# Optimization experiments

Measured on AMD Instinct MI355X. Metric: run time of the kernel, lower is better.

The kernel has to match this reference:

```python
import jax, jax.numpy as jnp
import numpy as np

T = 32.0                       # softmax temperature
THRESH = float(np.cos(np.pi * 40.0 / 180.0))  # cos(degree), degree=40
NEG_INF = -9.0e15


def setup_inputs() -> dict:
    key = jax.random.key(0)
    ks = jax.random.split(key, 11)
    B, C, D_IMG, D_ATT, H_ATT, H = 2048, 1000, 2048, 312, 128, 128
    def rn(k, shape, scale=1.0):
        return jax.random.normal(k, shape, dtype=jnp.float32) * scale
    return {
        "image_feats": rn(ks[0], (B, D_IMG)),
        "img_proto":   rn(ks[1], (C, D_IMG)),
        "attributes":  rn(ks[2], (C, D_ATT)),
        "unused":      0,
        # parameters
        "att_g":   rn(ks[3], (D_ATT, H_ATT), 0.05),
        "slim_w":  rn(ks[4], (D_IMG, D_ATT), 0.02),   # proto_slim weight (transposed torch layout)
        "slim_b":  rn(ks[5], (D_ATT,), 0.02),
        "img_w":   rn(ks[6], (D_IMG, H), 0.02),
        "proto_w": rn(ks[7], (2 * D_ATT, H), 0.02),   # att_dim + proto_red_dim = 624
        "proto_b": rn(ks[8], (1, H), 0.02),
        "fc_w":    rn(ks[9], (H, 1), 0.05),
        "fc_b":    rn(ks[10], (1,), 0.05),
    }


def reference(image_feats, img_proto, attributes, unused,
              att_g, slim_w, slim_b, img_w, proto_w, proto_b, fc_w, fc_b):
    # proto_slim: [C, D_img] -> [C, att_dim]
    proto_red = img_proto @ slim_w + slim_b

    # --- get_attention: cosine similarity among attribute projections ---
    g = attributes @ att_g                                   # [C, att_hC] (g == h in original)
    gn = g / jnp.clip(jnp.linalg.norm(g, axis=1, keepdims=True), 1e-12)
    sim = gn @ gn.T                                          # [C, C] cosine similarity
    raw = jnp.where(sim > THRESH, sim, NEG_INF)              # threshold mask
    attn = jax.nn.softmax(raw * T, axis=1)                   # [C, C]

    # --- propagate prototypes ---
    att_outs = attn @ attributes                             # [C, att_dim]
    img_proto_outs = attn @ proto_red                        # [C, att_dim]
    outs = jnp.concatenate([att_outs, img_proto_outs], axis=1)  # [C, 2*att_dim]

    # --- relation MLP (broadcast instead of materialized expand+matmul) ---
    img_h = image_feats @ img_w                              # [B, H]
    proto_h = outs @ proto_w                                 # [C, H]
    hidden = jax.nn.relu(img_h[:, None, :] + proto_h[None, :, :] + proto_b)  # [B, C, H]
    outputs = hidden @ fc_w + fc_b                           # [B, C, 1]
    return outputs[..., 0]                                   # [B, C]
```

## Files before the change

### kernel.cpp

```cpp
#include <hip/hip_runtime.h>

typedef unsigned short ushort_t;
typedef __bf16 bf16x8 __attribute__((ext_vector_type(8)));
typedef float f32x4 __attribute__((ext_vector_type(4)));
typedef float f32x2 __attribute__((ext_vector_type(2)));
typedef ushort_t us4 __attribute__((ext_vector_type(4)));

#define T_SOFT 32.0f
#define THRESH 0.76604444311897803f
#define SW 1048

__device__ __forceinline__ ushort_t f2bf(float f) {
  union { float f; unsigned u; } x; x.f = f;
  unsigned r = (x.u + 0x7fffu + ((x.u >> 16) & 1u)) >> 16;
  return (ushort_t)r;
}
__device__ __forceinline__ float bf2f(ushort_t h) {
  union { unsigned u; float f; } x; x.u = ((unsigned)h) << 16; return x.f;
}

__device__ __forceinline__ us4 pack4(float4 x) {
  union { unsigned u[2]; us4 h; } r;
  union { float4 f; unsigned u[4]; } a;
  a.f = x;
  r.u[0] = __builtin_amdgcn_perm(a.u[1] + 0x8000u, a.u[0] + 0x8000u, 0x07060302u);
  r.u[1] = __builtin_amdgcn_perm(a.u[3] + 0x8000u, a.u[2] + 0x8000u, 0x07060302u);
  return r.h;
}

__global__ __launch_bounds__(256) void tr3_k(const float* __restrict__ img_w, ushort_t* __restrict__ imgwT,
                                             const float* __restrict__ proto_w, ushort_t* __restrict__ protowT,
                                             const float* __restrict__ slim_w, ushort_t* __restrict__ slim_bf,
                                             const float* __restrict__ attributes, ushort_t* __restrict__ attr_bf,
                                             ushort_t* __restrict__ gn_bf,
                                             const float* __restrict__ slim_b, const float* __restrict__ proto_b,
                                             float* __restrict__ biasG) {
  int b = blockIdx.x, tid = threadIdx.x;
  if (b >= 336) {
    if (b < 496) {
      int t = (b - 336) * 256 + tid;
      int row = t / 20, c0 = (t - row * 20) * 16;
      #pragma unroll
      for (int g = 0; g < 4; ++g) {
        int c4 = c0 + g * 4;
        us4 v = {0, 0, 0, 0};
        if (c4 < 312) v = pack4(*reinterpret_cast<const float4*>(slim_w + (size_t)row * 312 + c4));
        *reinterpret_cast<us4*>(slim_bf + (size_t)row * 320 + c4) = v;
      }
    } else if (b < 576) {
      int t = (b - 496) * 256 + tid;
      int row = t / 20, c0 = (t - row * 20) * 16;
      #pragma unroll
      for (int g = 0; g < 4; ++g) {
        int c4 = c0 + g * 4;
        us4 v = {0, 0, 0, 0};
        if (row < 1000 && c4 < 312) v = pack4(*reinterpret_cast<const float4*>(attributes + (size_t)row * 312 + c4));
        *reinterpret_cast<us4*>(attr_bf + (size_t)row * 320 + c4) = v;
      }
    } else if (b == 576) {
      us4 z = {0, 0, 0, 0};
      *reinterpret_cast<us4*>(gn_bf + 1000 * 128 + tid * 4) = z;
    } else {
      int h = tid & 127;
      float acc = proto_b[h];
      for (int n = 0; n < 312; n += 4) {
        acc += slim_b[n + 0] * proto_w[(size_t)(312 + n) * 128 + h];
        acc += slim_b[n + 1] * proto_w[(size_t)(313 + n) * 128 + h];
        acc += slim_b[n + 2] * proto_w[(size_t)(314 + n) * 128 + h];
        acc += slim_b[n + 3] * proto_w[(size_t)(315 + n) * 128 + h];
      }
      if (tid < 128) biasG[h] = acc;
    }
    return;
  }
  __shared__ float tl[32][33];
  const float* src; ushort_t* dst; int R, C, Rpad, local;
  if (b < 256) { src = img_w;   dst = imgwT;   R = 2048; C = 128; Rpad = 2048; local = b;       }
  else         { src = proto_w; dst = protowT; R = 624;  C = 128; Rpad = 640;  local = b - 256; }
  int rt = local >> 2, ct = local & 3;
  int r0 = rt * 32, c0 = ct * 32;
  #pragma unroll
  for (int p = 0; p < 4; ++p) {
    int idx = p * 256 + tid;
    int rr = idx >> 5, cc = idx & 31;
    float v = 0.f;
    if (r0 + rr < R && c0 + cc < C) v = src[(size_t)(r0 + rr) * C + (c0 + cc)];
    tl[cc][rr] = v;
  }
  __syncthreads();
  int cc = tid >> 3, rq = tid & 7;
  us4 o;
  o[0] = f2bf(tl[cc][rq * 4 + 0]);
  o[1] = f2bf(tl[cc][rq * 4 + 1]);
  o[2] = f2bf(tl[cc][rq * 4 + 2]);
  o[3] = f2bf(tl[cc][rq * 4 + 3]);
  *reinterpret_cast<us4*>(dst + (size_t)(c0 + cc) * Rpad + r0 + rq * 4) = o;
}

__device__ __forceinline__ void gemm_imgh(const float* __restrict__ A, const ushort_t* __restrict__ BT,
                                          float* __restrict__ Cp, int r0, int k0,
                                          ushort_t* __restrict__ As, ushort_t* __restrict__ Bs, int tid) {
  const int SA = 72;
  int lane = tid & 63, wv = tid >> 6;
  int l15 = lane & 15, quad = lane >> 4;
  int arow = tid >> 4, akq = tid & 15;
  int brow = tid >> 3, bkq = tid & 7;
  const float* agp[8];
  #pragma unroll
  for (int p = 0; p < 8; ++p) agp[p] = A + (size_t)(r0 + arow + p * 16) * 2048 + k0 + akq * 4;
  const ushort_t* bgp[4];
  #pragma unroll
  for (int p = 0; p < 4; ++p) bgp[p] = BT + (size_t)(brow + p * 32) * 2048 + k0 + bkq * 8;

  float4 ap[8]; bf16x8 bp[4];
  #pragma unroll
  for (int p = 0; p < 8; ++p) ap[p] = *reinterpret_cast<const float4*>(agp[p]);
  #pragma unroll
  for (int p = 0; p < 4; ++p) bp[p] = *reinterpret_cast<const bf16x8*>(bgp[p]);

  f32x4 acc[2][8];
  #pragma unroll
  for (int i = 0; i < 2; ++i)
    #pragma unroll
    for (int j = 0; j < 8; ++j) acc[i][j] = f32x4{0.f, 0.f, 0.f, 0.f};

  for (int s = 0; s < 4; ++s) {
    if (s) __syncthreads();
    #pragma unroll
    for (int p = 0; p < 8; ++p)
      *reinterpret_cast<us4*>(As + (arow + p * 16) * SA + akq * 4) = pack4(ap[p]);
    #pragma unroll
    for (int p = 0; p < 4; ++p)
      *reinterpret_cast<bf16x8*>(Bs + (brow + p * 32) * SA + bkq * 8) = bp[p];
    if (s + 1 < 4) {
      #pragma unroll
      for (int p = 0; p < 8; ++p) ap[p] = *reinterpret_cast<const float4*>(agp[p] + 64);
      #pragma unroll
      for (int p = 0; p < 4; ++p) bp[p] = *reinterpret_cast<const bf16x8*>(bgp[p] + 64);
      #pragma unroll
      for (int p = 0; p < 8; ++p) agp[p] += 64;
      #pragma unroll
      for (int p = 0; p < 4; ++p) bgp[p] += 64;
    }
    __syncthreads();
    #pragma unroll
    for (int kh = 0; kh < 2; ++kh) {
      bf16x8 af[2];
      #pragma unroll
      for (int pi = 0; pi < 2; ++pi)
        af[pi] = *reinterpret_cast<bf16x8*>(As + ((wv * 2 + pi) * 16 + l15) * SA + kh * 32 + quad * 8);
      #pragma unroll
      for (int ct = 0; ct < 8; ++ct) {
        bf16x8 bfr = *reinterpret_cast<bf16x8*>(Bs + (ct * 16 + l15) * SA + kh * 32 + quad * 8);
        acc[0][ct] = __builtin_amdgcn_mfma_f32_16x16x32_bf16(af[0], bfr, acc[0][ct], 0, 0, 0);
        acc[1][ct] = __builtin_amdgcn_mfma_f32_16x16x32_bf16(af[1], bfr, acc[1][ct], 0, 0, 0);
      }
    }
  }
  #pragma unroll
  for (int pi = 0; pi < 2; ++pi)
    #pragma unroll
    for (int ct = 0; ct < 8; ++ct) {
      int col = ct * 16 + l15;
      #pragma unroll
      for (int r = 0; r < 4; ++r) {
        int row = r0 + (wv * 2 + pi) * 16 + quad * 4 + r;
        Cp[(size_t)row * 128 + col] = acc[pi][ct][r];
      }
    }
}

__device__ __forceinline__ void gemm_bb(const ushort_t* __restrict__ A, int sa,
                                        const ushort_t* __restrict__ B, int sb,
                                        int nsteps, ushort_t* __restrict__ As, ushort_t* __restrict__ Bs,
                                        int tid, f32x4 acc[2][8]) {
  const int SA = 72;
  int lane = tid & 63, wv = tid >> 6;
  int l15 = lane & 15, quad = lane >> 4;
  int hrow = tid >> 3, hkq = tid & 7;
  const ushort_t* ap = A + (size_t)hrow * sa + hkq * 8;
  const ushort_t* bp = B + (size_t)hrow * sb + hkq * 8;
  bf16x8 ar[4], br[4];
  #pragma unroll
  for (int p = 0; p < 4; ++p) {
    ar[p] = *reinterpret_cast<const bf16x8*>(ap + (size_t)p * 32 * sa);
    br[p] = *reinterpret_cast<const bf16x8*>(bp + (size_t)p * 32 * sb);
  }
  for (int s = 0; s < nsteps; ++s) {
    if (s) __syncthreads();
    #pragma unroll
    for (int p = 0; p < 4; ++p) {
      *reinterpret_cast<bf16x8*>(As + (hrow + p * 32) * SA + hkq * 8) = ar[p];
      *reinterpret_cast<bf16x8*>(Bs + (hrow + p * 32) * SA + hkq * 8) = br[p];
    }
    if (s + 1 < nsteps) {
      ap += 64; bp += 64;
      #pragma unroll
      for (int p = 0; p < 4; ++p) {
        ar[p] = *reinterpret_cast<const bf16x8*>(ap + (size_t)p * 32 * sa);
        br[p] = *reinterpret_cast<const bf16x8*>(bp + (size_t)p * 32 * sb);
      }
    }
    __syncthreads();
    #pragma unroll
    for (int kh = 0; kh < 2; ++kh) {
      bf16x8 af[2];
      #pragma unroll
      for (int pi = 0; pi < 2; ++pi)
        af[pi] = *reinterpret_cast<bf16x8*>(As + ((wv * 2 + pi) * 16 + l15) * SA + kh * 32 + quad * 8);
      #pragma unroll
      for (int ct = 0; ct < 8; ++ct) {
        bf16x8 bfr = *reinterpret_cast<bf16x8*>(Bs + (ct * 16 + l15) * SA + kh * 32 + quad * 8);
        acc[0][ct] = __builtin_amdgcn_mfma_f32_16x16x32_bf16(af[0], bfr, acc[0][ct], 0, 0, 0);
        acc[1][ct] = __builtin_amdgcn_mfma_f32_16x16x32_bf16(af[1], bfr, acc[1][ct], 0, 0, 0);
      }
    }
  }
}

__device__ __forceinline__ void gemm_b32(const ushort_t* __restrict__ A, int sa,
                                         const float* __restrict__ Bsrc, int sb, int brow0, int browmax,
                                         int nsteps, ushort_t* __restrict__ As, ushort_t* __restrict__ Bs,
                                         int tid, f32x4 acc[2][8]) {
  const int SA = 72;
  int lane = tid & 63, wv = tid >> 6;
  int l15 = lane & 15, quad = lane >> 4;
  int hrow = tid >> 3, hkq = tid & 7;
  int frow = tid >> 4, fkq = tid & 15;
  const ushort_t* ap = A + (size_t)hrow * sa + hkq * 8;
  const float* bgp[8];
  #pragma unroll
  for (int p = 0; p < 8; ++p) {
    int r = brow0 + frow + p * 16; if (r > browmax) r = browmax;
    bgp[p] = Bsrc + (size_t)r * sb + fkq * 4;
  }
  bf16x8 ar[4]; float4 brf[8];
  #pragma unroll
  for (int p = 0; p < 4; ++p) ar[p] = *reinterpret_cast<const bf16x8*>(ap + (size_t)p * 32 * sa);
  #pragma unroll
  for (int p = 0; p < 8; ++p) brf[p] = *reinterpret_cast<const float4*>(bgp[p]);
  for (int s = 0; s < nsteps; ++s) {
    if (s) __syncthreads();
    #pragma unroll
    for (int p = 0; p < 4; ++p)
      *reinterpret_cast<bf16x8*>(As + (hrow + p * 32) * SA + hkq * 8) = ar[p];
    #pragma unroll
    for (int p = 0; p < 8; ++p)
      *reinterpret_cast<us4*>(Bs + (frow + p * 16) * SA + fkq * 4) = pack4(brf[p]);
    if (s + 1 < nsteps) {
      ap += 64;
      #pragma unroll
      for (int p = 0; p < 4; ++p) ar[p] = *reinterpret_cast<const bf16x8*>(ap + (size_t)p * 32 * sa);
      #pragma unroll
      for (int p = 0; p < 8; ++p) { bgp[p] += 64; brf[p] = *reinterpret_cast<const float4*>(bgp[p]); }
    }
    __syncthreads();
    #pragma unroll
    for (int kh = 0; kh < 2; ++kh) {
      bf16x8 af[2];
      #pragma unroll
      for (int pi = 0; pi < 2; ++pi)
        af[pi] = *reinterpret_cast<bf16x8*>(As + ((wv * 2 + pi) * 16 + l15) * SA + kh * 32 + quad * 8);
      #pragma unroll
      for (int ct = 0; ct < 8; ++ct) {
        bf16x8 bfr = *reinterpret_cast<bf16x8*>(Bs + (ct * 16 + l15) * SA + kh * 32 + quad * 8);
        acc[0][ct] = __builtin_amdgcn_mfma_f32_16x16x32_bf16(af[0], bfr, acc[0][ct], 0, 0, 0);
        acc[1][ct] = __builtin_amdgcn_mfma_f32_16x16x32_bf16(af[1], bfr, acc[1][ct], 0, 0, 0);
      }
    }
  }
}

__global__ __launch_bounds__(256) void mega_k(
    const float* __restrict__ attributes, const float* __restrict__ att_g,
    ushort_t* __restrict__ gn_bf,
    const float* __restrict__ image_feats, const ushort_t* __restrict__ imgwT,
    float* __restrict__ ihp,
    const ushort_t* __restrict__ protowT, const ushort_t* __restrict__ slim_bf,
    ushort_t* __restrict__ M2T) {
  __shared__ ushort_t As[128 * 72];
  __shared__ ushort_t Bs[128 * 72];
  int b = blockIdx.x, tid = threadIdx.x;
  if (b < 125) {
    __shared__ float a_lds[8][316];
    __shared__ float red2[8][2];
    int h = tid & 127;
    int c0 = b * 8;
    for (int idx = tid; idx < 8 * 312; idx += 256) {
      int r = idx / 312;
      int k = idx - r * 312;
      a_lds[r][k] = attributes[(c0 + r) * 312 + k];
    }
    __syncthreads();
    float acc[8] = {0.f,0.f,0.f,0.f,0.f,0.f,0.f,0.f};
    #pragma unroll 2
    for (int k = 0; k < 312; k += 4) {
      float w0 = att_g[(k + 0) * 128 + h];
      float w1 = att_g[(k + 1) * 128 + h];
      float w2 = att_g[(k + 2) * 128 + h];
      float w3 = att_g[(k + 3) * 128 + h];
      #pragma unroll
      for (int r = 0; r < 8; ++r) {
        float4 a4 = *reinterpret_cast<const float4*>(&a_lds[r][k]);
        acc[r] += a4.x * w0 + a4.y * w1 + a4.z * w2 + a4.w * w3;
      }
    }
    int lane = tid & 63, wvid = (tid >> 6) & 1;
    #pragma unroll
    for (int r = 0; r < 8; ++r) {
      float v = acc[r] * acc[r];
      #pragma unroll
      for (int off = 32; off > 0; off >>= 1) v += __shfl_xor(v, off, 64);
      if (lane == 0) red2[r][wvid] = v;
    }
    __syncthreads();
    #pragma unroll
    for (int r = 0; r < 8; ++r) {
      float nrm = fmaxf(sqrtf(red2[r][0] + red2[r][1]), 1e-12f);
      gn_bf[(c0 + r) * 128 + h] = f2bf(acc[r] / nrm);
    }
    return;
  }
  b -= 125;
  if (b < 128) {
    int tile = b >> 3, kc = b & 7;
    gemm_imgh(image_feats, imgwT, ihp + (size_t)kc * 2048 * 128, tile * 128, kc * 256, As, Bs, tid);
    return;
  }
  b -= 128;
  int c0 = b * 128;
  f32x4 acc[2][8];
  #pragma unroll
  for (int i = 0; i < 2; ++i)
    #pragma unroll
    for (int j = 0; j < 8; ++j) acc[i][j] = f32x4{0.f, 0.f, 0.f, 0.f};
  gemm_bb(protowT + 312, 640, slim_bf + (size_t)c0 * 320, 320, 5, As, Bs, tid, acc);
  int lane = tid & 63, wv = tid >> 6;
  int l15 = lane & 15, quad = lane >> 4;
  #pragma unroll
  for (int pi = 0; pi < 2; ++pi)
    #pragma unroll
    for (int ct = 0; ct < 8; ++ct) {
      int col = c0 + ct * 16 + l15;
      #pragma unroll
      for (int r = 0; r < 4; ++r) {
        int row = (wv * 2 + pi) * 16 + quad * 4 + r;
        M2T[(size_t)row * 2048 + col] = f2bf(acc[pi][ct][r]);
      }
    }
}

__global__ __launch_bounds__(256) void k3_k(
    const float* __restrict__ ihp, float* __restrict__ img_h,
    const ushort_t* __restrict__ protowT, const ushort_t* __restrict__ M2T,
    const ushort_t* __restrict__ attr_bf, const float* __restrict__ img_proto,
    float* __restrict__ GT_part) {
  __shared__ ushort_t As[128 * 72];
  __shared__ ushort_t Bs[128 * 72];
  int b = blockIdx.x, tid = threadIdx.x;
  if (b < 64) {
    int t = b * 256 + tid;
    size_t base = (size_t)t * 16;
    #pragma unroll
    for (int g = 0; g < 4; ++g) {
      float4 s = *reinterpret_cast<const float4*>(ihp + base + g * 4);
      #pragma unroll
      for (int c = 1; c < 8; ++c) {
        float4 v = *reinterpret_cast<const float4*>(ihp + (size_t)c * 262144 + base + g * 4);
        s.x += v.x; s.y += v.y; s.z += v.z; s.w += v.w;
      }
      *reinterpret_cast<float4*>(img_h + base + g * 4) = s;
    }
    return;
  }
  int q = b - 64;
  int jt = q / 5, ch = q - jt * 5;
  int j0 = jt * 128;
  f32x4 acc[2][8];
  #pragma unroll
  for (int i = 0; i < 2; ++i)
    #pragma unroll
    for (int j = 0; j < 8; ++j) acc[i][j] = f32x4{0.f, 0.f, 0.f, 0.f};
  if (ch == 0) {
    gemm_bb(protowT, 640, attr_bf + (size_t)j0 * 320, 320, 5, As, Bs, tid, acc);
  } else {
    int k0 = (ch - 1) * 512;
    gemm_b32(M2T + k0, 2048, img_proto + k0, 2048, j0, 999, 8, As, Bs, tid, acc);
  }
  int lane = tid & 63, wv = tid >> 6;
  int l15 = lane & 15, quad = lane >> 4;
  float* dst = GT_part + (size_t)ch * 128 * 1024;
  #pragma unroll
  for (int pi = 0; pi < 2; ++pi)
    #pragma unroll
    for (int ct = 0; ct < 8; ++ct) {
      int col = j0 + ct * 16 + l15;
      #pragma unroll
      for (int r = 0; r < 4; ++r) {
        int row = (wv * 2 + pi) * 16 + quad * 4 + r;
        dst[(size_t)row * 1024 + col] = acc[pi][ct][r];
      }
    }
}

__global__ __launch_bounds__(256) void k4_k(const float* __restrict__ GT_part,
                                            const float* __restrict__ biasG,
                                            ushort_t* __restrict__ GT) {
  int t = blockIdx.x * 256 + threadIdx.x;
  size_t base = (size_t)t * 16;
  int row = (int)(base >> 10);
  float bg = biasG[row];
  #pragma unroll
  for (int g = 0; g < 4; ++g) {
    float4 s = *reinterpret_cast<const float4*>(GT_part + base + g * 4);
    #pragma unroll
    for (int c = 1; c < 5; ++c) {
      float4 v = *reinterpret_cast<const float4*>(GT_part + (size_t)c * 131072 + base + g * 4);
      s.x += v.x; s.y += v.y; s.z += v.z; s.w += v.w;
    }
    s.x += bg; s.y += bg; s.z += bg; s.w += bg;
    *reinterpret_cast<us4*>(GT + base + g * 4) = pack4(s);
  }
}

__global__ __launch_bounds__(256) void attn5_k(
    const ushort_t* __restrict__ gn_bf, const ushort_t* __restrict__ GT,
    float* __restrict__ ph) {
  __shared__ ushort_t W[16 * SW];
  __shared__ float rsum[16];
  __shared__ int flags[63];
  int tid = threadIdx.x;
  int i0 = blockIdx.x * 16;
  int lane = tid & 63, wv = tid >> 6;
  int l15 = lane & 15, quad = lane >> 4;
  if (tid < 63) flags[tid] = 0;
  if (tid >= 64 && tid < 80) rsum[tid - 64] = 0.f;
  W[(tid >> 4) * SW + 1008 + (tid & 15)] = 0;
  __syncthreads();

  const ushort_t* abase = gn_bf + (size_t)(i0 + l15) * 128 + quad * 8;
  bf16x8 af0 = *reinterpret_cast<const bf16x8*>(abase);
  bf16x8 af1 = *reinterpret_cast<const bf16x8*>(abase + 32);
  bf16x8 af2 = *reinterpret_cast<const bf16x8*>(abase + 64);
  bf16x8 af3 = *reinterpret_cast<const bf16x8*>(abase + 96);
  float rs[4] = {0.f, 0.f, 0.f, 0.f};
  for (int jt = wv; jt < 63; jt += 4) {
    const ushort_t* bbase = gn_bf + (size_t)(jt * 16 + l15) * 128 + quad * 8;
    f32x4 d = {0.f, 0.f, 0.f, 0.f};
    d = __builtin_amdgcn_mfma_f32_16x16x32_bf16(af0, *reinterpret_cast<const bf16x8*>(bbase),      d, 0, 0, 0);
    d = __builtin_amdgcn_mfma_f32_16x16x32_bf16(af1, *reinterpret_cast<const bf16x8*>(bbase + 32), d, 0, 0, 0);
    d = __builtin_amdgcn_mfma_f32_16x16x32_bf16(af2, *reinterpret_cast<const bf16x8*>(bbase + 64), d, 0, 0, 0);
    d = __builtin_amdgcn_mfma_f32_16x16x32_bf16(af3, *reinterpret_cast<const bf16x8*>(bbase + 96), d, 0, 0, 0);
    int hot = 0;
    #pragma unroll
    for (int r = 0; r < 4; ++r) {
      float w = 0.f;
      if (d[r] > THRESH) { w = __expf(T_SOFT * (d[r] - 1.0f)); hot = 1; }
      ushort_t wb = f2bf(w);
      W[(quad * 4 + r) * SW + jt * 16 + l15] = wb;
      rs[r] += bf2f(wb);
    }
    if (hot) flags[jt] = 1;
  }
  #pragma unroll
  for (int r = 0; r < 4; ++r) {
    float v = rs[r];
    v += __shfl_xor(v, 1, 64); v += __shfl_xor(v, 2, 64);
    v += __shfl_xor(v, 4, 64); v += __shfl_xor(v, 8, 64);
    if (l15 == 0) atomicAdd(&rsum[quad * 4 + r], v);
  }
  __syncthreads();

  f32x4 acc2[2];
  acc2[0] = f32x4{0.f, 0.f, 0.f, 0.f};
  acc2[1] = f32x4{0.f, 0.f, 0.f, 0.f};
  for (int s = 0; s < 32; ++s) {
    int f = flags[2 * s] | ((2 * s + 1 < 63) ? flags[2 * s + 1] : 0);
    if (!f) continue;
    bf16x8 a = *reinterpret_cast<bf16x8*>(W + l15 * SW + s * 32 + quad * 8);
    #pragma unroll
    for (int t = 0; t < 2; ++t) {
      int h = (wv * 2 + t) * 16 + l15;
      bf16x8 bfr = *reinterpret_cast<const bf16x8*>(GT + (size_t)h * 1024 + s * 32 + quad * 8);
      acc2[t] = __builtin_amdgcn_mfma_f32_16x16x32_bf16(a, bfr, acc2[t], 0, 0, 0);
    }
  }
  #pragma unroll
  for (int t = 0; t < 2; ++t) {
    int h = (wv * 2 + t) * 16 + l15;
    #pragma unroll
    for (int r = 0; r < 4; ++r) {
      int row = quad * 4 + r;
      int gi = i0 + row;
      float inv = 1.f / fmaxf(rsum[row], 1e-30f);
      if (gi < 1000) ph[(size_t)gi * 128 + h] = acc2[t][r] * inv;
    }
  }
}

__global__ __launch_bounds__(512) void final_k(
    const float* __restrict__ img_h, const float* __restrict__ ph,
    const float* __restrict__ fc_w, const float* __restrict__ fc_b,
    float* __restrict__ out) {
  __shared__ float ih[128][132];
  __shared__ float ps[64][132];
  __shared__ float ws_[128];
  int tid = threadIdx.x;
  int b0 = blockIdx.x * 128;
  int c0 = blockIdx.y * 64;
  for (int idx = tid; idx < 4096; idx += 512) {
    int row = idx >> 5, c4 = (idx & 31) * 4;
    float4 v = *reinterpret_cast<const float4*>(img_h + (size_t)(b0 + row) * 128 + c4);
    *reinterpret_cast<float4*>(&ih[row][c4]) = v;
  }
  for (int idx = tid; idx < 2048; idx += 512) {
    int row = idx >> 5, c4 = (idx & 31) * 4;
    int c = c0 + row;
    float4 v = make_float4(0.f, 0.f, 0.f, 0.f);
    if (c < 1000) v = *reinterpret_cast<const float4*>(ph + (size_t)c * 128 + c4);
    *reinterpret_cast<float4*>(&ps[row][c4]) = v;
  }
  if (tid < 128) ws_[tid] = fc_w[tid];
  __syncthreads();
  int tx = tid & 15, ty = tid >> 4;
  f32x2 acc[4][4] = {};
  const f32x2 zero2 = {0.f, 0.f};
  for (int h = 0; h < 128; h += 4) {
    float4 w4 = *reinterpret_cast<float4*>(&ws_[h]);
    f32x2 wlo = {w4.x, w4.y}, whi = {w4.z, w4.w};
    float4 a4[4], p4[4];
    #pragma unroll
    for (int i = 0; i < 4; ++i) a4[i] = *reinterpret_cast<float4*>(&ih[ty * 4 + i][h]);
    #pragma unroll
    for (int j = 0; j < 4; ++j) p4[j] = *reinterpret_cast<float4*>(&ps[tx * 4 + j][h]);
    #pragma unroll
    for (int i = 0; i < 4; ++i) {
      f32x2 alo = {a4[i].x, a4[i].y}, ahi = {a4[i].z, a4[i].w};
      #pragma unroll
      for (int j = 0; j < 4; ++j) {
        f32x2 plo = {p4[j].x, p4[j].y}, phi = {p4[j].z, p4[j].w};
        f32x2 t0 = __builtin_elementwise_max(alo + plo, zero2);
        f32x2 t1 = __builtin_elementwise_max(ahi + phi, zero2);
        acc[i][j] = acc[i][j] + t0 * wlo;
        acc[i][j] = acc[i][j] + t1 * whi;
      }
    }
  }
  float fb = fc_b[0];
  #pragma unroll
  for (int i = 0; i < 4; ++i) {
    int b = b0 + ty * 4 + i;
    int c = c0 + tx * 4;
    if (c < 1000) {
      float4 v = make_float4(acc[i][0].x + acc[i][0].y + fb, acc[i][1].x + acc[i][1].y + fb,
                             acc[i][2].x + acc[i][2].y + fb, acc[i][3].x + acc[i][3].y + fb);
      *reinterpret_cast<float4*>(out + (size_t)b * 1000 + c) = v;
    }
  }
}

extern "C" void kernel_launch(void* const* d_in, const int* in_sizes, int n_in,
                              void* d_out, int out_size, void* d_ws, size_t ws_size,
                              hipStream_t stream) {
  const float* image_feats = (const float*)d_in[0];
  const float* img_proto   = (const float*)d_in[1];
  const float* attributes  = (const float*)d_in[2];
  const float* att_g   = (const float*)d_in[4];
  const float* slim_w  = (const float*)d_in[5];
  const float* slim_b  = (const float*)d_in[6];
  const float* img_w   = (const float*)d_in[7];
  const float* proto_w = (const float*)d_in[8];
  const float* proto_b = (const float*)d_in[9];
  const float* fc_w    = (const float*)d_in[10];
  const float* fc_b    = (const float*)d_in[11];
  float* out = (float*)d_out;

  char* ws = (char*)d_ws;
  size_t o = 0;
  auto alloc = [&](size_t bytes) { size_t r = o; o += (bytes + 255) & ~(size_t)255; return r; };
  ushort_t* imgwT   = (ushort_t*)(ws + alloc(128ull * 2048 * 2));
  ushort_t* protowT = (ushort_t*)(ws + alloc(128ull * 640 * 2));
  ushort_t* slim_bf = (ushort_t*)(ws + alloc(2048ull * 320 * 2));
  ushort_t* attr_bf = (ushort_t*)(ws + alloc(1024ull * 320 * 2));
  ushort_t* gn_bf   = (ushort_t*)(ws + alloc(1008ull * 128 * 2));
  ushort_t* M2T     = (ushort_t*)(ws + alloc(128ull * 2048 * 2));
  ushort_t* GT      = (ushort_t*)(ws + alloc(128ull * 1024 * 2));
  float* biasG     = (float*)(ws + alloc(128ull * 4));
  float* ihp       = (float*)(ws + alloc(8ull * 2048 * 128 * 4));
  float* GT_part   = (float*)(ws + alloc(5ull * 128 * 1024 * 4));
  float* img_h     = (float*)(ws + alloc(2048ull * 128 * 4));
  float* ph        = (float*)(ws + alloc(1000ull * 128 * 4));

  tr3_k<<<578, 256, 0, stream>>>(img_w, imgwT, proto_w, protowT, slim_w, slim_bf,
                                 attributes, attr_bf, gn_bf, slim_b, proto_b, biasG);

  mega_k<<<269, 256, 0, stream>>>(attributes, att_g, gn_bf,
                                  image_feats, imgwT, ihp, protowT, slim_bf, M2T);

  k3_k<<<104, 256, 0, stream>>>(ihp, img_h, protowT, M2T, attr_bf, img_proto, GT_part);

  k4_k<<<32, 256, 0, stream>>>(GT_part, biasG, GT);

  attn5_k<<<63, 256, 0, stream>>>(gn_bf, GT, ph);

  final_k<<<dim3(16, 16), 512, 0, stream>>>(img_h, ph, fc_w, fc_b, out);
}
```

Baseline: 169.9 us.

## Fold weight transpose/convert into GEMM staging and drop the separate prep kernel

Removes the standalone transpose/bf16 conversion kernel by having each GEMM convert fp32 weights and activations to bf16 while staging them into shared memory. The attributes@proto_w GEMM moves into the first kernel, and the partial-sum grids of the reduction kernel are reshaped. The attention kernel goes to 512 threads with one MFMA tile per wave, and the final kernel uses smaller 256-thread blocks for more parallelism. This saves a launch and the intermediate bf16 copies, at the cost of redoing the fp32-to-bf16 conversion inside each GEMM block, including strided transposed loads.

Measured after the change: 169.0 us. Within noise of the previous version (-0.5%).

```diff
diff --git a/kernel.cpp b/kernel.cpp
--- a/kernel.cpp
+++ b/kernel.cpp
@@ -9,6 +9,7 @@
 #define T_SOFT 32.0f
 #define THRESH 0.76604444311897803f
 #define SW 1048
+#define SA 72
 
 __device__ __forceinline__ ushort_t f2bf(float f) {
   union { float f; unsigned u; } x; x.f = f;
@@ -28,258 +29,84 @@
   return r.h;
 }
 
-__global__ __launch_bounds__(256) void tr3_k(const float* __restrict__ img_w, ushort_t* __restrict__ imgwT,
-                                             const float* __restrict__ proto_w, ushort_t* __restrict__ protowT,
-                                             const float* __restrict__ slim_w, ushort_t* __restrict__ slim_bf,
-                                             const float* __restrict__ attributes, ushort_t* __restrict__ attr_bf,
-                                             ushort_t* __restrict__ gn_bf,
-                                             const float* __restrict__ slim_b, const float* __restrict__ proto_b,
-                                             float* __restrict__ biasG) {
-  int b = blockIdx.x, tid = threadIdx.x;
-  if (b >= 336) {
-    if (b < 496) {
-      int t = (b - 336) * 256 + tid;
-      int row = t / 20, c0 = (t - row * 20) * 16;
-      #pragma unroll
-      for (int g = 0; g < 4; ++g) {
-        int c4 = c0 + g * 4;
-        us4 v = {0, 0, 0, 0};
-        if (c4 < 312) v = pack4(*reinterpret_cast<const float4*>(slim_w + (size_t)row * 312 + c4));
-        *reinterpret_cast<us4*>(slim_bf + (size_t)row * 320 + c4) = v;
-      }
-    } else if (b < 576) {
-      int t = (b - 496) * 256 + tid;
-      int row = t / 20, c0 = (t - row * 20) * 16;
-      #pragma unroll
-      for (int g = 0; g < 4; ++g) {
-        int c4 = c0 + g * 4;
-        us4 v = {0, 0, 0, 0};
-        if (row < 1000 && c4 < 312) v = pack4(*reinterpret_cast<const float4*>(attributes + (size_t)row * 312 + c4));
-        *reinterpret_cast<us4*>(attr_bf + (size_t)row * 320 + c4) = v;
-      }
-    } else if (b == 576) {
-      us4 z = {0, 0, 0, 0};
-      *reinterpret_cast<us4*>(gn_bf + 1000 * 128 + tid * 4) = z;
-    } else {
-      int h = tid & 127;
-      float acc = proto_b[h];
-      for (int n = 0; n < 312; n += 4) {
-        acc += slim_b[n + 0] * proto_w[(size_t)(312 + n) * 128 + h];
-        acc += slim_b[n + 1] * proto_w[(size_t)(313 + n) * 128 + h];
-        acc += slim_b[n + 2] * proto_w[(size_t)(314 + n) * 128 + h];
-        acc += slim_b[n + 3] * proto_w[(size_t)(315 + n) * 128 + h];
-      }
-      if (tid < 128) biasG[h] = acc;
-    }
-    return;
-  }
-  __shared__ float tl[32][33];
-  const float* src; ushort_t* dst; int R, C, Rpad, local;
-  if (b < 256) { src = img_w;   dst = imgwT;   R = 2048; C = 128; Rpad = 2048; local = b;       }
-  else         { src = proto_w; dst = protowT; R = 624;  C = 128; Rpad = 640;  local = b - 256; }
-  int rt = local >> 2, ct = local & 3;
-  int r0 = rt * 32, c0 = ct * 32;
-  #pragma unroll
-  for (int p = 0; p < 4; ++p) {
-    int idx = p * 256 + tid;
-    int rr = idx >> 5, cc = idx & 31;
-    float v = 0.f;
-    if (r0 + rr < R && c0 + cc < C) v = src[(size_t)(r0 + rr) * C + (c0 + cc)];
-    tl[cc][rr] = v;
-  }
-  __syncthreads();
-  int cc = tid >> 3, rq = tid & 7;
-  us4 o;
-  o[0] = f2bf(tl[cc][rq * 4 + 0]);
-  o[1] = f2bf(tl[cc][rq * 4 + 1]);
-  o[2] = f2bf(tl[cc][rq * 4 + 2]);
-  o[3] = f2bf(tl[cc][rq * 4 + 3]);
-  *reinterpret_cast<us4*>(dst + (size_t)(c0 + cc) * Rpad + r0 + rq * 4) = o;
-}
-
-__device__ __forceinline__ void gemm_imgh(const float* __restrict__ A, const ushort_t* __restrict__ BT,
-                                          float* __restrict__ Cp, int r0, int k0,
-                                          ushort_t* __restrict__ As, ushort_t* __restrict__ Bs, int tid) {
-  const int SA = 72;
+__device__ __forceinline__ void stage_T(const float* __restrict__ src, int srs, int rbase, int rlimit,
+                                        int nbase, ushort_t* __restrict__ dst, int tid) {
+  int kg = (tid >> 4) * 4;
+  int ns = (tid & 15) * 8;
+  float v[4][8];
+  #pragma unroll
+  for (int i = 0; i < 4; ++i) {
+    int r = rbase + kg + i;
+    float4 a = make_float4(0.f,0.f,0.f,0.f), c = make_float4(0.f,0.f,0.f,0.f);
+    if (r < rlimit) {
+      a = *reinterpret_cast<const float4*>(src + (size_t)r * srs + nbase + ns);
+      c = *reinterpret_cast<const float4*>(src + (size_t)r * srs + nbase + ns + 4);
+    }
+    v[i][0]=a.x; v[i][1]=a.y; v[i][2]=a.z; v[i][3]=a.w;
+    v[i][4]=c.x; v[i][5]=c.y; v[i][6]=c.z; v[i][7]=c.w;
+  }
+  #pragma unroll
+  for (int j = 0; j < 8; ++j) {
+    us4 o;
+    o[0] = f2bf(v[0][j]); o[1] = f2bf(v[1][j]); o[2] = f2bf(v[2][j]); o[3] = f2bf(v[3][j]);
+    *reinterpret_cast<us4*>(dst + (size_t)(ns + j) * SA + kg) = o;
+  }
+}
+
+__device__ __forceinline__ void stage_R(const float* __restrict__ src, int srs, int rowbase, int rowmax,
+                                        int kbase, int climit, ushort_t* __restrict__ dst, int tid) {
+  int frow = tid >> 4;
+  int fk = (tid & 15) * 4;
+  #pragma unroll
+  for (int p = 0; p < 8; ++p) {
+    int row = rowbase + frow + p * 16; if (row > rowmax) row = rowmax;
+    int k = kbase + fk;
+    float4 val = make_float4(0.f,0.f,0.f,0.f);
+    if (k < climit) val = *reinterpret_cast<const float4*>(src + (size_t)row * srs + k);
+    *reinterpret_cast<us4*>(dst + (size_t)(frow + p * 16) * SA + fk) = pack4(val);
+  }
+}
+
+__device__ __forceinline__ void stage_Abf(const ushort_t* __restrict__ src, int srs, int kbase,
+                                          ushort_t* __restrict__ dst, int tid) {
+  int hrow = tid >> 3;
+  int hk = (tid & 7) * 8;
+  #pragma unroll
+  for (int p = 0; p < 4; ++p)
+    *reinterpret_cast<bf16x8*>(dst + (size_t)(hrow + p * 32) * SA + hk) =
+      *reinterpret_cast<const bf16x8*>(src + (size_t)(hrow + p * 32) * srs + kbase + hk);
+}
+
+__device__ __forceinline__ void mfma8(ushort_t* __restrict__ As, ushort_t* __restrict__ Bs,
+                                      int tid, f32x4 acc[2][8]) {
   int lane = tid & 63, wv = tid >> 6;
   int l15 = lane & 15, quad = lane >> 4;
-  int arow = tid >> 4, akq = tid & 15;
-  int brow = tid >> 3, bkq = tid & 7;
-  const float* agp[8];
-  #pragma unroll
-  for (int p = 0; p < 8; ++p) agp[p] = A + (size_t)(r0 + arow + p * 16) * 2048 + k0 + akq * 4;
-  const ushort_t* bgp[4];
-  #pragma unroll
-  for (int p = 0; p < 4; ++p) bgp[p] = BT + (size_t)(brow + p * 32) * 2048 + k0 + bkq * 8;
-
-  float4 ap[8]; bf16x8 bp[4];
-  #pragma unroll
-  for (int p = 0; p < 8; ++p) ap[p] = *reinterpret_cast<const float4*>(agp[p]);
-  #pragma unroll
-  for (int p = 0; p < 4; ++p) bp[p] = *reinterpret_cast<const bf16x8*>(bgp[p]);
-
-  f32x4 acc[2][8];
-  #pragma unroll
-  for (int i = 0; i < 2; ++i)
-    #pragma unroll
-    for (int j = 0; j < 8; ++j) acc[i][j] = f32x4{0.f, 0.f, 0.f, 0.f};
-
-  for (int s = 0; s < 4; ++s) {
-    if (s) __syncthreads();
-    #pragma unroll
-    for (int p = 0; p < 8; ++p)
-      *reinterpret_cast<us4*>(As + (arow + p * 16) * SA + akq * 4) = pack4(ap[p]);
-    #pragma unroll
-    for (int p = 0; p < 4; ++p)
-      *reinterpret_cast<bf16x8*>(Bs + (brow + p * 32) * SA + bkq * 8) = bp[p];
-    if (s + 1 < 4) {
-      #pragma unroll
-      for (int p = 0; p < 8; ++p) ap[p] = *reinterpret_cast<const float4*>(agp[p] + 64);
-      #pragma unroll
-      for (int p = 0; p < 4; ++p) bp[p] = *reinterpret_cast<const bf16x8*>(bgp[p] + 64);
-      #pragma unroll
-      for (int p = 0; p < 8; ++p) agp[p] += 64;
-      #pragma unroll
-      for (int p = 0; p < 4; ++p) bgp[p] += 64;
-    }
-    __syncthreads();
-    #pragma unroll
-    for (int kh = 0; kh < 2; ++kh) {
-      bf16x8 af[2];
-      #pragma unroll
-      for (int pi = 0; pi < 2; ++pi)
-        af[pi] = *reinterpret_cast<bf16x8*>(As + ((wv * 2 + pi) * 16 + l15) * SA + kh * 32 + quad * 8);
-      #pragma unroll
-      for (int ct = 0; ct < 8; ++ct) {
-        bf16x8 bfr = *reinterpret_cast<bf16x8*>(Bs + (ct * 16 + l15) * SA + kh * 32 + quad * 8);
-        acc[0][ct] = __builtin_amdgcn_mfma_f32_16x16x32_bf16(af[0], bfr, acc[0][ct], 0, 0, 0);
-        acc[1][ct] = __builtin_amdgcn_mfma_f32_16x16x32_bf16(af[1], bfr, acc[1][ct], 0, 0, 0);
-      }
-    }
-  }
-  #pragma unroll
-  for (int pi = 0; pi < 2; ++pi)
+  #pragma unroll
+  for (int kh = 0; kh < 2; ++kh) {
+    bf16x8 af[2];
+    #pragma unroll
+    for (int pi = 0; pi < 2; ++pi)
+      af[pi] = *reinterpret_cast<bf16x8*>(As + ((wv * 2 + pi) * 16 + l15) * SA + kh * 32 + quad * 8);
     #pragma unroll
     for (int ct = 0; ct < 8; ++ct) {
-      int col = ct * 16 + l15;
-      #pragma unroll
-      for (int r = 0; r < 4; ++r) {
-        int row = r0 + (wv * 2 + pi) * 16 + quad * 4 + r;
-        Cp[(size_t)row * 128 + col] = acc[pi][ct][r];
-      }
-    }
-}
-
-__device__ __forceinline__ void gemm_bb(const ushort_t* __restrict__ A, int sa,
-                                        const ushort_t* __restrict__ B, int sb,
-                                        int nsteps, ushort_t* __restrict__ As, ushort_t* __restrict__ Bs,
-                                        int tid, f32x4 acc[2][8]) {
-  const int SA = 72;
-  int lane = tid & 63, wv = tid >> 6;
-  int l15 = lane & 15, quad = lane >> 4;
-  int hrow = tid >> 3, hkq = tid & 7;
-  const ushort_t* ap = A + (size_t)hrow * sa + hkq * 8;
-  const ushort_t* bp = B + (size_t)hrow * sb + hkq * 8;
-  bf16x8 ar[4], br[4];
-  #pragma unroll
-  for (int p = 0; p < 4; ++p) {
-    ar[p] = *reinterpret_cast<const bf16x8*>(ap + (size_t)p * 32 * sa);
-    br[p] = *reinterpret_cast<const bf16x8*>(bp + (size_t)p * 32 * sb);
-  }
-  for (int s = 0; s < nsteps; ++s) {
-    if (s) __syncthreads();
-    #pragma unroll
-    for (int p = 0; p < 4; ++p) {
-      *reinterpret_cast<bf16x8*>(As + (hrow + p * 32) * SA + hkq * 8) = ar[p];
-      *reinterpret_cast<bf16x8*>(Bs + (hrow + p * 32) * SA + hkq * 8) = br[p];
-    }
-    if (s + 1 < nsteps) {
-      ap += 64; bp += 64;
-      #pragma unroll
-      for (int p = 0; p < 4; ++p) {
-        ar[p] = *reinterpret_cast<const bf16x8*>(ap + (size_t)p * 32 * sa);
-        br[p] = *reinterpret_cast<const bf16x8*>(bp + (size_t)p * 32 * sb);
-      }
-    }
-    __syncthreads();
-    #pragma unroll
-    for (int kh = 0; kh < 2; ++kh) {
-      bf16x8 af[2];
-      #pragma unroll
-      for (int pi = 0; pi < 2; ++pi)
-        af[pi] = *reinterpret_cast<bf16x8*>(As + ((wv * 2 + pi) * 16 + l15) * SA + kh * 32 + quad * 8);
-      #pragma unroll
-      for (int ct = 0; ct < 8; ++ct) {
-        bf16x8 bfr = *reinterpret_cast<bf16x8*>(Bs + (ct * 16 + l15) * SA + kh * 32 + quad * 8);
-        acc[0][ct] = __builtin_amdgcn_mfma_f32_16x16x32_bf16(af[0], bfr, acc[0][ct], 0, 0, 0);
-        acc[1][ct] = __builtin_amdgcn_mfma_f32_16x16x32_bf16(af[1], bfr, acc[1][ct], 0, 0, 0);
-      }
-    }
-  }
-}
-
-__device__ __forceinline__ void gemm_b32(const ushort_t* __restrict__ A, int sa,
-                                         const float* __restrict__ Bsrc, int sb, int brow0, int browmax,
-                                         int nsteps, ushort_t* __restrict__ As, ushort_t* __restrict__ Bs,
-                                         int tid, f32x4 acc[2][8]) {
-  const int SA = 72;
-  int lane = tid & 63, wv = tid >> 6;
-  int l15 = lane & 15, quad = lane >> 4;
-  int hrow = tid >> 3, hkq = tid & 7;
-  int frow = tid >> 4, fkq = tid & 15;
-  const ushort_t* ap = A + (size_t)hrow * sa + hkq * 8;
-  const float* bgp[8];
-  #pragma unroll
-  for (int p = 0; p < 8; ++p) {
-    int r = brow0 + frow + p * 16; if (r > browmax) r = browmax;
-    bgp[p] = Bsrc + (size_t)r * sb + fkq * 4;
-  }
-  bf16x8 ar[4]; float4 brf[8];
-  #pragma unroll
-  for (int p = 0; p < 4; ++p) ar[p] = *reinterpret_cast<const bf16x8*>(ap + (size_t)p * 32 * sa);
-  #pragma unroll
-  for (int p = 0; p < 8; ++p) brf[p] = *reinterpret_cast<const float4*>(bgp[p]);
-  for (int s = 0; s < nsteps; ++s) {
-    if (s) __syncthreads();
-    #pragma unroll
-    for (int p = 0; p < 4; ++p)
-      *reinterpret_cast<bf16x8*>(As + (hrow + p * 32) * SA + hkq * 8) = ar[p];
-    #pragma unroll
-    for (int p = 0; p < 8; ++p)
-      *reinterpret_cast<us4*>(Bs + (frow + p * 16) * SA + fkq * 4) = pack4(brf[p]);
-    if (s + 1 < nsteps) {
-      ap += 64;
-      #pragma unroll
-      for (int p = 0; p < 4; ++p) ar[p] = *reinterpret_cast<const bf16x8*>(ap + (size_t)p * 32 * sa);
-      #pragma unroll
-      for (int p = 0; p < 8; ++p) { bgp[p] += 64; brf[p] = *reinterpret_cast<const float4*>(bgp[p]); }
-    }
-    __syncthreads();
-    #pragma unroll
-    for (int kh = 0; kh < 2; ++kh) {
-      bf16x8 af[2];
-      #pragma unroll
-      for (int pi = 0; pi < 2; ++pi)
-        af[pi] = *reinterpret_cast<bf16x8*>(As + ((wv * 2 + pi) * 16 + l15) * SA + kh * 32 + quad * 8);
-      #pragma unroll
-      for (int ct = 0; ct < 8; ++ct) {
-        bf16x8 bfr = *reinterpret_cast<bf16x8*>(Bs + (ct * 16 + l15) * SA + kh * 32 + quad * 8);
-        acc[0][ct] = __builtin_amdgcn_mfma_f32_16x16x32_bf16(af[0], bfr, acc[0][ct], 0, 0, 0);
-        acc[1][ct] = __builtin_amdgcn_mfma_f32_16x16x32_bf16(af[1], bfr, acc[1][ct], 0, 0, 0);
-      }
-    }
-  }
-}
-
-__global__ __launch_bounds__(256) void mega_k(
+      bf16x8 bfr = *reinterpret_cast<bf16x8*>(Bs + (ct * 16 + l15) * SA + kh * 32 + quad * 8);
+      acc[0][ct] = __builtin_amdgcn_mfma_f32_16x16x32_bf16(af[0], bfr, acc[0][ct], 0, 0, 0);
+      acc[1][ct] = __builtin_amdgcn_mfma_f32_16x16x32_bf16(af[1], bfr, acc[1][ct], 0, 0, 0);
+    }
+  }
+}
+
+__global__ __launch_bounds__(256) void prep_k(
     const float* __restrict__ attributes, const float* __restrict__ att_g,
     ushort_t* __restrict__ gn_bf,
-    const float* __restrict__ image_feats, const ushort_t* __restrict__ imgwT,
+    const float* __restrict__ image_feats, const float* __restrict__ img_w,
     float* __restrict__ ihp,
-    const ushort_t* __restrict__ protowT, const ushort_t* __restrict__ slim_bf,
-    ushort_t* __restrict__ M2T) {
-  __shared__ ushort_t As[128 * 72];
-  __shared__ ushort_t Bs[128 * 72];
+    const float* __restrict__ proto_w, const float* __restrict__ slim_w,
+    ushort_t* __restrict__ M2T, float* __restrict__ GT_part,
+    const float* __restrict__ slim_b, const float* __restrict__ proto_b,
+    float* __restrict__ biasG) {
+  __shared__ ushort_t As[128 * SA];
+  __shared__ ushort_t Bs[128 * SA];
   int b = blockIdx.x, tid = threadIdx.x;
   if (b < 125) {
     __shared__ float a_lds[8][316];
@@ -321,48 +148,113 @@
     }
     return;
   }
-  b -= 125;
-  if (b < 128) {
-    int tile = b >> 3, kc = b & 7;
-    gemm_imgh(image_feats, imgwT, ihp + (size_t)kc * 2048 * 128, tile * 128, kc * 256, As, Bs, tid);
-    return;
-  }
-  b -= 128;
-  int c0 = b * 128;
-  f32x4 acc[2][8];
-  #pragma unroll
-  for (int i = 0; i < 2; ++i)
-    #pragma unroll
-    for (int j = 0; j < 8; ++j) acc[i][j] = f32x4{0.f, 0.f, 0.f, 0.f};
-  gemm_bb(protowT + 312, 640, slim_bf + (size_t)c0 * 320, 320, 5, As, Bs, tid, acc);
+  if (b == 125) {
+    us4 z = {0, 0, 0, 0};
+    *reinterpret_cast<us4*>(gn_bf + 1000 * 128 + tid * 4) = z;
+    return;
+  }
+  if (b == 126) {
+    int h = tid & 127;
+    float acc = proto_b[h];
+    for (int n = 0; n < 312; n += 4) {
+      acc += slim_b[n + 0] * proto_w[(size_t)(312 + n) * 128 + h];
+      acc += slim_b[n + 1] * proto_w[(size_t)(313 + n) * 128 + h];
+      acc += slim_b[n + 2] * proto_w[(size_t)(314 + n) * 128 + h];
+      acc += slim_b[n + 3] * proto_w[(size_t)(315 + n) * 128 + h];
+    }
+    if (tid < 128) biasG[h] = acc;
+    return;
+  }
   int lane = tid & 63, wv = tid >> 6;
   int l15 = lane & 15, quad = lane >> 4;
-  #pragma unroll
-  for (int pi = 0; pi < 2; ++pi)
-    #pragma unroll
-    for (int ct = 0; ct < 8; ++ct) {
-      int col = c0 + ct * 16 + l15;
-      #pragma unroll
-      for (int r = 0; r < 4; ++r) {
-        int row = (wv * 2 + pi) * 16 + quad * 4 + r;
-        M2T[(size_t)row * 2048 + col] = f2bf(acc[pi][ct][r]);
-      }
-    }
-}
-
-__global__ __launch_bounds__(256) void k3_k(
+  f32x4 acc[2][8];
+  #pragma unroll
+  for (int i = 0; i < 2; ++i)
+    #pragma unroll
+    for (int j = 0; j < 8; ++j) acc[i][j] = f32x4{0.f, 0.f, 0.f, 0.f};
+
+  if (b < 255) {
+    int q = b - 127;
+    int tile = q >> 3, kc = q & 7;
+    int r0 = tile * 128, k0 = kc * 256;
+    for (int s = 0; s < 4; ++s) {
+      if (s) __syncthreads();
+      stage_R(image_feats, 2048, r0, 2047, k0 + s * 64, 1 << 30, As, tid);
+      stage_T(img_w, 128, k0 + s * 64, 2048, 0, Bs, tid);
+      __syncthreads();
+      mfma8(As, Bs, tid, acc);
+    }
+    float* Cp = ihp + (size_t)kc * 2048 * 128;
+    #pragma unroll
+    for (int pi = 0; pi < 2; ++pi)
+      #pragma unroll
+      for (int ct = 0; ct < 8; ++ct) {
+        int col = ct * 16 + l15;
+        #pragma unroll
+        for (int r = 0; r < 4; ++r) {
+          int row = r0 + (wv * 2 + pi) * 16 + quad * 4 + r;
+          Cp[(size_t)row * 128 + col] = acc[pi][ct][r];
+        }
+      }
+    return;
+  }
+  if (b < 271) {
+    int c0 = (b - 255) * 128;
+    for (int s = 0; s < 5; ++s) {
+      if (s) __syncthreads();
+      stage_T(proto_w, 128, 312 + s * 64, 624, 0, As, tid);
+      stage_R(slim_w, 312, c0, 2047, s * 64, 312, Bs, tid);
+      __syncthreads();
+      mfma8(As, Bs, tid, acc);
+    }
+    #pragma unroll
+    for (int pi = 0; pi < 2; ++pi)
+      #pragma unroll
+      for (int ct = 0; ct < 8; ++ct) {
+        int col = c0 + ct * 16 + l15;
+        #pragma unroll
+        for (int r = 0; r < 4; ++r) {
+          int row = (wv * 2 + pi) * 16 + quad * 4 + r;
+          M2T[(size_t)row * 2048 + col] = f2bf(acc[pi][ct][r]);
+        }
+      }
+    return;
+  }
+  {
+    int j0 = (b - 271) * 128;
+    for (int s = 0; s < 5; ++s) {
+      if (s) __syncthreads();
+      stage_T(proto_w, 128, s * 64, 312, 0, As, tid);
+      stage_R(attributes, 312, j0, 999, s * 64, 312, Bs, tid);
+      __syncthreads();
+      mfma8(As, Bs, tid, acc);
+    }
+    #pragma unroll
+    for (int pi = 0; pi < 2; ++pi)
+      #pragma unroll
+      for (int ct = 0; ct < 8; ++ct) {
+        int col = j0 + ct * 16 + l15;
+        #pragma unroll
+        for (int r = 0; r < 4; ++r) {
+          int row = (wv * 2 + pi) * 16 + quad * 4 + r;
+          GT_part[(size_t)row * 1024 + col] = acc[pi][ct][r];
+        }
+      }
+  }
+}
+
+__global__ __launch_bounds__(256) void red_k(
     const float* __restrict__ ihp, float* __restrict__ img_h,
-    const ushort_t* __restrict__ protowT, const ushort_t* __restrict__ M2T,
-    const ushort_t* __restrict__ attr_bf, const float* __restrict__ img_proto,
+    const ushort_t* __restrict__ M2T, const float* __restrict__ img_proto,
     float* __restrict__ GT_part) {
-  __shared__ ushort_t As[128 * 72];
-  __shared__ ushort_t Bs[128 * 72];
+  __shared__ ushort_t As[128 * SA];
+  __shared__ ushort_t Bs[128 * SA];
   int b = blockIdx.x, tid = threadIdx.x;
-  if (b < 64) {
+  if (b < 128) {
     int t = b * 256 + tid;
-    size_t base = (size_t)t * 16;
-    #pragma unroll
-    for (int g = 0; g < 4; ++g) {
+    size_t base = (size_t)t * 8;
+    #pragma unroll
+    for (int g = 0; g < 2; ++g) {
       float4 s = *reinterpret_cast<const float4*>(ihp + base + g * 4);
       #pragma unroll
       for (int c = 1; c < 8; ++c) {
@@ -373,23 +265,24 @@
     }
     return;
   }
-  int q = b - 64;
-  int jt = q / 5, ch = q - jt * 5;
-  int j0 = jt * 128;
+  int q = b - 128;
+  int jt = q >> 2, ch = q & 3;
+  int j0 = jt * 128, k0 = ch * 512;
   f32x4 acc[2][8];
   #pragma unroll
   for (int i = 0; i < 2; ++i)
     #pragma unroll
     for (int j = 0; j < 8; ++j) acc[i][j] = f32x4{0.f, 0.f, 0.f, 0.f};
-  if (ch == 0) {
-    gemm_bb(protowT, 640, attr_bf + (size_t)j0 * 320, 320, 5, As, Bs, tid, acc);
-  } else {
-    int k0 = (ch - 1) * 512;
-    gemm_b32(M2T + k0, 2048, img_proto + k0, 2048, j0, 999, 8, As, Bs, tid, acc);
+  for (int s = 0; s < 8; ++s) {
+    if (s) __syncthreads();
+    stage_Abf(M2T, 2048, k0 + s * 64, As, tid);
+    stage_R(img_proto, 2048, j0, 999, k0 + s * 64, 1 << 30, Bs, tid);
+    __syncthreads();
+    mfma8(As, Bs, tid, acc);
   }
   int lane = tid & 63, wv = tid >> 6;
   int l15 = lane & 15, quad = lane >> 4;
-  float* dst = GT_part + (size_t)ch * 128 * 1024;
+  float* dst = GT_part + (size_t)(ch + 1) * 131072;
   #pragma unroll
   for (int pi = 0; pi < 2; ++pi)
     #pragma unroll
@@ -403,9 +296,9 @@
     }
 }
 
-__global__ __launch_bounds__(256) void k4_k(const float* __restrict__ GT_part,
-                                            const float* __restrict__ biasG,
-                                            ushort_t* __restrict__ GT) {
+__global__ __launch_bounds__(256) void gtred_k(const float* __restrict__ GT_part,
+                                               const float* __restrict__ biasG,
+                                               ushort_t* __restrict__ GT) {
   int t = blockIdx.x * 256 + threadIdx.x;
   size_t base = (size_t)t * 16;
   int row = (int)(base >> 10);
@@ -423,7 +316,7 @@
   }
 }
 
-__global__ __launch_bounds__(256) void attn5_k(
+__global__ __launch_bounds__(512) void attn6_k(
     const ushort_t* __restrict__ gn_bf, const ushort_t* __restrict__ GT,
     float* __restrict__ ph) {
   __shared__ ushort_t W[16 * SW];
@@ -435,7 +328,7 @@
   int l15 = lane & 15, quad = lane >> 4;
   if (tid < 63) flags[tid] = 0;
   if (tid >= 64 && tid < 80) rsum[tid - 64] = 0.f;
-  W[(tid >> 4) * SW + 1008 + (tid & 15)] = 0;
+  if (tid < 256) W[(tid >> 4) * SW + 1008 + (tid & 15)] = 0;
   __syncthreads();
 
   const ushort_t* abase = gn_bf + (size_t)(i0 + l15) * 128 + quad * 8;
@@ -444,7 +337,7 @@
   bf16x8 af2 = *reinterpret_cast<const bf16x8*>(abase + 64);
   bf16x8 af3 = *reinterpret_cast<const bf16x8*>(abase + 96);
   float rs[4] = {0.f, 0.f, 0.f, 0.f};
-  for (int jt = wv; jt < 63; jt += 4) {
+  for (int jt = wv; jt < 63; jt += 8) {
     const ushort_t* bbase = gn_bf + (size_t)(jt * 16 + l15) * 128 + quad * 8;
     f32x4 d = {0.f, 0.f, 0.f, 0.f};
     d = __builtin_amdgcn_mfma_f32_16x16x32_bf16(af0, *reinterpret_cast<const bf16x8*>(bbase),      d, 0, 0, 0);
@@ -471,49 +364,40 @@
   }
   __syncthreads();
 
-  f32x4 acc2[2];
-  acc2[0] = f32x4{0.f, 0.f, 0.f, 0.f};
-  acc2[1] = f32x4{0.f, 0.f, 0.f, 0.f};
+  f32x4 acc2 = {0.f, 0.f, 0.f, 0.f};
+  int h = wv * 16 + l15;
   for (int s = 0; s < 32; ++s) {
     int f = flags[2 * s] | ((2 * s + 1 < 63) ? flags[2 * s + 1] : 0);
     if (!f) continue;
     bf16x8 a = *reinterpret_cast<bf16x8*>(W + l15 * SW + s * 32 + quad * 8);
-    #pragma unroll
-    for (int t = 0; t < 2; ++t) {
-      int h = (wv * 2 + t) * 16 + l15;
-      bf16x8 bfr = *reinterpret_cast<const bf16x8*>(GT + (size_t)h * 1024 + s * 32 + quad * 8);
-      acc2[t] = __builtin_amdgcn_mfma_f32_16x16x32_bf16(a, bfr, acc2[t], 0, 0, 0);
-    }
-  }
-  #pragma unroll
-  for (int t = 0; t < 2; ++t) {
-    int h = (wv * 2 + t) * 16 + l15;
-    #pragma unroll
-    for (int r = 0; r < 4; ++r) {
-      int row = quad * 4 + r;
-      int gi = i0 + row;
-      float inv = 1.f / fmaxf(rsum[row], 1e-30f);
-      if (gi < 1000) ph[(size_t)gi * 128 + h] = acc2[t][r] * inv;
-    }
-  }
-}
-
-__global__ __launch_bounds__(512) void final_k(
+    bf16x8 bfr = *reinterpret_cast<const bf16x8*>(GT + (size_t)h * 1024 + s * 32 + quad * 8);
+    acc2 = __builtin_amdgcn_mfma_f32_16x16x32_bf16(a, bfr, acc2, 0, 0, 0);
+  }
+  #pragma unroll
+  for (int r = 0; r < 4; ++r) {
+    int row = quad * 4 + r;
+    int gi = i0 + row;
+    float inv = 1.f / fmaxf(rsum[row], 1e-30f);
+    if (gi < 1000) ph[(size_t)gi * 128 + h] = acc2[r] * inv;
+  }
+}
+
+__global__ __launch_bounds__(256) void final_k(
     const float* __restrict__ img_h, const float* __restrict__ ph,
     const float* __restrict__ fc_w, const float* __restrict__ fc_b,
     float* __restrict__ out) {
-  __shared__ float ih[128][132];
+  __shared__ float ih[64][132];
   __shared__ float ps[64][132];
   __shared__ float ws_[128];
   int tid = threadIdx.x;
-  int b0 = blockIdx.x * 128;
+  int b0 = blockIdx.x * 64;
   int c0 = blockIdx.y * 64;
-  for (int idx = tid; idx < 4096; idx += 512) {
+  for (int idx = tid; idx < 2048; idx += 256) {
     int row = idx >> 5, c4 = (idx & 31) * 4;
     float4 v = *reinterpret_cast<const float4*>(img_h + (size_t)(b0 + row) * 128 + c4);
     *reinterpret_cast<float4*>(&ih[row][c4]) = v;
   }
-  for (int idx = tid; idx < 2048; idx += 512) {
+  for (int idx = tid; idx < 2048; idx += 256) {
     int row = idx >> 5, c4 = (idx & 31) * 4;
     int c = c0 + row;
     float4 v = make_float4(0.f, 0.f, 0.f, 0.f);
@@ -578,10 +462,6 @@
   char* ws = (char*)d_ws;
   size_t o = 0;
   auto alloc = [&](size_t bytes) { size_t r = o; o += (bytes + 255) & ~(size_t)255; return r; };
-  ushort_t* imgwT   = (ushort_t*)(ws + alloc(128ull * 2048 * 2));
-  ushort_t* protowT = (ushort_t*)(ws + alloc(128ull * 640 * 2));
-  ushort_t* slim_bf = (ushort_t*)(ws + alloc(2048ull * 320 * 2));
-  ushort_t* attr_bf = (ushort_t*)(ws + alloc(1024ull * 320 * 2));
   ushort_t* gn_bf   = (ushort_t*)(ws + alloc(1008ull * 128 * 2));
   ushort_t* M2T     = (ushort_t*)(ws + alloc(128ull * 2048 * 2));
   ushort_t* GT      = (ushort_t*)(ws + alloc(128ull * 1024 * 2));
@@ -591,17 +471,16 @@
   float* img_h     = (float*)(ws + alloc(2048ull * 128 * 4));
   float* ph        = (float*)(ws + alloc(1000ull * 128 * 4));
 
-  tr3_k<<<578, 256, 0, stream>>>(img_w, imgwT, proto_w, protowT, slim_w, slim_bf,
-                                 attributes, attr_bf, gn_bf, slim_b, proto_b, biasG);
-
-  mega_k<<<269, 256, 0, stream>>>(attributes, att_g, gn_bf,
-                                  image_feats, imgwT, ihp, protowT, slim_bf, M2T);
-
-  k3_k<<<104, 256, 0, stream>>>(ihp, img_h, protowT, M2T, attr_bf, img_proto, GT_part);
-
-  k4_k<<<32, 256, 0, stream>>>(GT_part, biasG, GT);
-
-  attn5_k<<<63, 256, 0, stream>>>(gn_bf, GT, ph);
-
-  final_k<<<dim3(16, 16), 512, 0, stream>>>(img_h, ph, fc_w, fc_b, out);
-}
+  prep_k<<<279, 256, 0, stream>>>(attributes, att_g, gn_bf,
+                                  image_feats, img_w, ihp,
+                                  proto_w, slim_w, M2T, GT_part,
+                                  slim_b, proto_b, biasG);
+
+  red_k<<<160, 256, 0, stream>>>(ihp, img_h, M2T, img_proto, GT_part);
+
+  gtred_k<<<32, 256, 0, stream>>>(GT_part, biasG, GT);
+
+  attn6_k<<<63, 512, 0, stream>>>(gn_bf, GT, ph);
+
+  final_k<<<dim3(32, 16), 256, 0, stream>>>(img_h, ph, fc_w, fc_b, out);
+}
```
